# Kernel optimization log

Hardware: AMD Instinct MI355X
Metric: run time of the kernel (lower is better)

The kernel has to match this reference:

```python
import jax, jax.numpy as jnp
import numpy as np

B, D, V = 1024, 512, 100000
M = 0.4
EPS = 1e-07


def setup_inputs() -> dict:
    key = jax.random.key(0)
    k1, k2, k3 = jax.random.split(key, 3)
    inp = jax.random.normal(k1, (B, D), dtype=jnp.float32)
    # xavier_uniform for (D, V): limit = sqrt(6/(D+V))
    limit = float(np.sqrt(6.0 / (D + V)))
    weight = jax.random.uniform(k2, (D, V), dtype=jnp.float32, minval=-limit, maxval=limit)
    labels = jax.random.randint(k3, (B,), 0, V, dtype=jnp.int64)
    return {"input": inp, "weight": weight, "labels": labels}


def reference(input, weight, labels):
    # L2-normalize rows of input and columns of weight (F.normalize eps=1e-12)
    x_norm = input / jnp.maximum(jnp.linalg.norm(input, axis=1, keepdims=True), 1e-12)
    w_norm = weight / jnp.maximum(jnp.linalg.norm(weight, axis=0, keepdims=True), 1e-12)
    cosine = x_norm @ w_norm                                # [B, V]
    cosine = jnp.clip(cosine, -1.0 + EPS, 1.0 - EPS)
    arcos = jnp.arccos(cosine)
    # add margin m only at the label class (one-hot add without dense one-hot)
    rows = jnp.arange(B)
    arcos = arcos.at[rows, labels].add(M)
    logits = jnp.cos(arcos)                                 # [B, V]
    # cross-entropy, mean reduction
    logz = jax.nn.logsumexp(logits, axis=1)                 # [B]
    label_logit = logits[rows, labels]                      # [B]
    loss = jnp.mean(logz - label_logit)
    return loss
```

## Files before the change

kernel.cpp:

```cpp
#include <hip/hip_runtime.h>
#include <math.h>

#define B_    1024
#define D_    512
#define V_    100000
#define NP_   100096
#define NT_   782
#define EPS_  1e-7f
#define COSM  0.9210609940028851f
#define SINM  0.3894183423086505f

typedef __bf16 bf16x8 __attribute__((ext_vector_type(8)));
typedef float  f32x4  __attribute__((ext_vector_type(4)));

struct alignas(16) US8 { unsigned short h[8]; };

__device__ __forceinline__ unsigned short f2bf(float f) {
  union { float f; unsigned u; } a; a.f = f;
  unsigned u = a.u;
  u += 0x7FFFu + ((u >> 16) & 1u);
  return (unsigned short)(u >> 16);
}

__device__ __forceinline__ void async_copy16(void* lds, const void* g) {
  __builtin_amdgcn_global_load_lds(
      (const __attribute__((address_space(1))) void*)g,
      (__attribute__((address_space(3))) void*)lds, 16, 0, 0);
}

__global__ void x_prep(const float* __restrict__ x,
                       unsigned short* __restrict__ xb,
                       float* __restrict__ S) {
  int t = threadIdx.x;
  int lane = t & 63, wave = t >> 6;
  int row = blockIdx.x * 4 + wave;
  const float* xr = x + (size_t)row * D_;
  f32x4 a = *(const f32x4*)(xr + lane * 8);
  f32x4 b = *(const f32x4*)(xr + lane * 8 + 4);
  float ss = a[0]*a[0] + a[1]*a[1] + a[2]*a[2] + a[3]*a[3]
           + b[0]*b[0] + b[1]*b[1] + b[2]*b[2] + b[3]*b[3];
#pragma unroll
  for (int off = 32; off > 0; off >>= 1) ss += __shfl_xor(ss, off, 64);
  float inv = 1.0f / fmaxf(sqrtf(ss), 1e-12f);
  US8 pk;
#pragma unroll
  for (int j = 0; j < 4; ++j) pk.h[j]     = f2bf(a[j] * inv);
#pragma unroll
  for (int j = 0; j < 4; ++j) pk.h[4 + j] = f2bf(b[j] * inv);
  *(US8*)(xb + (size_t)row * D_ + lane * 8) = pk;
  if (lane == 0) S[row] = 0.0f;
}

#define WPC 64
#define KH  256

__global__ __launch_bounds__(256) void w_prep(const float* __restrict__ w,
                                              unsigned short* __restrict__ wbT,
                                              float* __restrict__ wssq) {
  __shared__ US8  T16[WPC][32];
  __shared__ float sq[16][WPC];
  int t = threadIdx.x;
  int c0 = blockIdx.x * WPC;
  int qv = t & 15;
  int rg = t >> 4;
  int colv = qv * 4;
  int lane = t & 63, wave = t >> 6;
  bool vok = (c0 + colv + 3) < V_;
  float ssq[4] = {0.0f, 0.0f, 0.0f, 0.0f};

  for (int h = 0; h < 2; ++h) {
#pragma unroll
    for (int o = 0; o < 2; ++o) {
      int kc = rg * 2 + o;
      int rowb = h * KH + kc * 8;
      US8 pk[4] = {};
      if (vok) {
#pragma unroll
        for (int i = 0; i < 8; ++i) {
          f32x4 v = *(const f32x4*)(w + (size_t)(rowb + i) * V_ + c0 + colv);
#pragma unroll
          for (int cc = 0; cc < 4; ++cc) {
            ssq[cc] += v[cc] * v[cc];
            pk[cc].h[i] = f2bf(v[cc]);
          }
        }
      }
#pragma unroll
      for (int cc = 0; cc < 4; ++cc)
        T16[colv + cc][kc ^ qv] = pk[cc];
    }
    __syncthreads();
#pragma unroll
    for (int ci = 0; ci < 8; ++ci) {
      int col = wave * 16 + ci * 2 + (lane >> 5);
      int kc = lane & 31;
      US8 pk = T16[col][kc ^ (col >> 2)];
      *(US8*)(wbT + (size_t)(c0 + col) * D_ + h * KH + kc * 8) = pk;
    }
    __syncthreads();
  }

#pragma unroll
  for (int cc = 0; cc < 4; ++cc) sq[rg][colv + cc] = ssq[cc];
  __syncthreads();
  if (t < WPC && (c0 + t) < V_) {
    float tot = 0.0f;
#pragma unroll
    for (int p = 0; p < 16; ++p) tot += sq[p][t];
    wssq[c0 + t] = tot;
  }
}

#define BM 256
#define BN 128
#define BK 64
#define NKT (D_ / BK)

__global__ __launch_bounds__(512, 4) void gemm_fused_dma(
    const unsigned short* __restrict__ xb,
    const unsigned short* __restrict__ wbT,
    const float* __restrict__ wssq,
    const int* __restrict__ labels,
    float* __restrict__ S, float* __restrict__ Lb) {
  int bid = blockIdx.x;
  int xcd = bid & 7;
  int slot = bid >> 3;
  int tm = slot & 3;
  int tn = xcd * 98 + (slot >> 2);
  if (tn >= NT_) return;
  int m0 = tm * BM, n0 = tn * BN;

  __shared__ unsigned short Ab[BM * BK];
  __shared__ unsigned short Bb[BN * BK];
  __shared__ int labT[BM];
  int t = threadIdx.x;
  if (t < BM) labT[t] = labels[m0 + t];
  int lane = t & 63;
  int q = lane >> 4, l15 = lane & 15;
  int wave = t >> 6;
  int wm = (wave & 3) * 64, wn = (wave >> 2) * 64;
  f32x4 acc[4][4] = {};

  const unsigned short* gA[4]; unsigned short* lA[4];
  const unsigned short* gB[2]; unsigned short* lB[2];
#pragma unroll
  for (int j = 0; j < 4; ++j) {
    int p = t + 512 * j;
    int m = p >> 3;
    int kc = (p & 7) ^ (m & 7);
    gA[j] = xb + (size_t)(m0 + m) * D_ + kc * 8;
    lA[j] = Ab + p * 8;
  }
#pragma unroll
  for (int j = 0; j < 2; ++j) {
    int p = t + 512 * j;
    int m = p >> 3;
    int kc = (p & 7) ^ (m & 7);
    gB[j] = wbT + (size_t)(n0 + m) * D_ + kc * 8;
    lB[j] = Bb + p * 8;
  }

  int h = l15 & 7;
  for (int kt = 0; kt < D_; kt += BK) {
#pragma unroll
    for (int j = 0; j < 4; ++j) async_copy16(lA[j], gA[j] + kt);
#pragma unroll
    for (int j = 0; j < 2; ++j) async_copy16(lB[j], gB[j] + kt);
    __syncthreads();

#pragma unroll
    for (int s = 0; s < 2; ++s) {
      int kx = s * 4 + q;
      bf16x8 af[4], bfr[4];
#pragma unroll
      for (int ri = 0; ri < 4; ++ri) {
        int row_ = wm + ri * 16 + l15;
        af[ri] = *(const bf16x8*)&Ab[(row_ * 8 + (kx ^ h)) * 8];
      }
#pragma unroll
      for (int ci = 0; ci < 4; ++ci) {
        int row_ = wn + ci * 16 + l15;
        bfr[ci] = *(const bf16x8*)&Bb[(row_ * 8 + (kx ^ h)) * 8];
      }
#pragma unroll
      for (int ri = 0; ri < 4; ++ri)
#pragma unroll
        for (int ci = 0; ci < 4; ++ci)
          acc[ri][ci] = __builtin_amdgcn_mfma_f32_16x16x32_bf16(
              af[ri], bfr[ci], acc[ri][ci], 0, 0, 0);
    }
    __syncthreads();
  }

  float iw[4]; int vcol[4];
#pragma unroll
  for (int ci = 0; ci < 4; ++ci) {
    int nl = wn + ci * 16 + l15;
    vcol[ci] = n0 + nl;
    iw[ci] = (vcol[ci] < V_) ? 1.0f / fmaxf(sqrtf(wssq[vcol[ci]]), 1e-12f)
                             : 0.0f;
  }
#pragma unroll
  for (int ri = 0; ri < 4; ++ri) {
#pragma unroll
    for (int reg = 0; reg < 4; ++reg) {
      int ml = wm + ri * 16 + q * 4 + reg;
      int r = m0 + ml;
      int lab = labT[ml];
      float s = 0.0f;
#pragma unroll
      for (int ci = 0; ci < 4; ++ci) {
        float cv = acc[ri][ci][reg] * iw[ci];
        cv = fminf(fmaxf(cv, -1.0f + EPS_), 1.0f - EPS_);
        float logit = cv;
        if (vcol[ci] == lab) {
          logit = cv * COSM - sqrtf(fmaxf(1.0f - cv * cv, 0.0f)) * SINM;
          Lb[r] = logit;
        }
        s += (vcol[ci] < V_) ? __expf(logit) : 0.0f;
      }
      s += __shfl_xor(s, 1, 64);
      s += __shfl_xor(s, 2, 64);
      s += __shfl_xor(s, 4, 64);
      s += __shfl_xor(s, 8, 64);
      if (l15 == 0) atomicAdd(&S[r], s);
    }
  }
}

__global__ __launch_bounds__(256) void gemm_fused_inline(
    const unsigned short* __restrict__ xb,
    const float* __restrict__ w,
    const int* __restrict__ labels,
    float* __restrict__ S, float* __restrict__ Lb) {
  int bid = blockIdx.x;
  int xcd = bid & 7;
  int slot = bid >> 3;
  int tn = xcd * 98 + (slot >> 3);
  int tm = slot & 7;
  if (tn >= NT_) return;
  int m0 = tm * 128, n0 = tn * 128;

  __shared__ unsigned short Ab[128 * 64];
  __shared__ unsigned short Bb[128 * 64];
  __shared__ float sqred[8][128];
  __shared__ float iwL[128];
  __shared__ int labT[128];
  int t = threadIdx.x;
  if (t < 128) labT[t] = labels[m0 + t];
  int lane = t & 63;
  int q = lane >> 4, l15 = lane & 15;
  int wave = t >> 6;
  int wm = (wave & 1) * 64, wn = (wave >> 1) * 64;
  f32x4 acc[4][4] = {};

  const unsigned short* gA[4];
  unsigned short* lA[4];
#pragma unroll
  for (int j = 0; j < 4; ++j) {
    int p = t + 256 * j;
    int m = p >> 3;
    int kc = (p & 7) ^ (m & 7);
    gA[j] = xb + (size_t)(m0 + m) * D_ + kc * 8;
    lA[j] = Ab + p * 8;
  }

  int cg = t & 31;
  int rp = t >> 5;
  int c0l = cg * 4;
  bool vok = (n0 + c0l + 3) < V_;
  const float* wbase = w + (size_t)rp * 8 * V_ + n0 + c0l;
  unsigned short* bdst[4];
#pragma unroll
  for (int cc = 0; cc < 4; ++cc) {
    int col = c0l + cc;
    bdst[cc] = &Bb[(col * 8 + (rp ^ (col & 7))) * 8];
  }
  float ssq[4] = {0.0f, 0.0f, 0.0f, 0.0f};

  for (int kt = 0; kt < D_; kt += 64) {
#pragma unroll
    for (int j = 0; j < 4; ++j) async_copy16(lA[j], gA[j] + kt);

    f32x4 row[8];
    if (vok) {
#pragma unroll
      for (int i = 0; i < 8; ++i)
        row[i] = *(const f32x4*)(wbase + (size_t)i * V_);
    } else {
#pragma unroll
      for (int i = 0; i < 8; ++i) row[i] = f32x4{0.0f, 0.0f, 0.0f, 0.0f};
    }
#pragma unroll
    for (int cc = 0; cc < 4; ++cc) {
      US8 pk;
#pragma unroll
      for (int i = 0; i < 8; ++i) {
        float v = row[i][cc];
        ssq[cc] += v * v;
        pk.h[i] = f2bf(v);
      }
      *(US8*)bdst[cc] = pk;
    }
    wbase += (size_t)64 * V_;

    __syncthreads();
    int h = l15 & 7;
#pragma unroll
    for (int s = 0; s < 2; ++s) {
      int kx = s * 4 + q;
      bf16x8 af[4], bfr[4];
#pragma unroll
      for (int ri = 0; ri < 4; ++ri) {
        int row_ = wm + ri * 16 + l15;
        af[ri] = *(const bf16x8*)&Ab[(row_ * 8 + (kx ^ h)) * 8];
      }
#pragma unroll
      for (int ci = 0; ci < 4; ++ci) {
        int row_ = wn + ci * 16 + l15;
        bfr[ci] = *(const bf16x8*)&Bb[(row_ * 8 + (kx ^ h)) * 8];
      }
#pragma unroll
      for (int ri = 0; ri < 4; ++ri)
#pragma unroll
        for (int ci = 0; ci < 4; ++ci)
          acc[ri][ci] = __builtin_amdgcn_mfma_f32_16x16x32_bf16(
              af[ri], bfr[ci], acc[ri][ci], 0, 0, 0);
    }
    __syncthreads();
  }

#pragma unroll
  for (int cc = 0; cc < 4; ++cc) sqred[rp][c0l + cc] = ssq[cc];
  __syncthreads();
  if (t < 128) {
    float tot = 0.0f;
#pragma unroll
    for (int p = 0; p < 8; ++p) tot += sqred[p][t];
    iwL[t] = ((n0 + t) < V_) ? 1.0f / fmaxf(sqrtf(tot), 1e-12f) : 0.0f;
  }
  __syncthreads();

  float iw[4]; int vcol[4];
#pragma unroll
  for (int ci = 0; ci < 4; ++ci) {
    int nl = wn + ci * 16 + l15;
    vcol[ci] = n0 + nl;
    iw[ci] = iwL[nl];
  }
#pragma unroll
  for (int ri = 0; ri < 4; ++ri) {
#pragma unroll
    for (int reg = 0; reg < 4; ++reg) {
      int ml = wm + ri * 16 + q * 4 + reg;
      int r = m0 + ml;
      int lab = labT[ml];
      float s = 0.0f;
#pragma unroll
      for (int ci = 0; ci < 4; ++ci) {
        float cv = acc[ri][ci][reg] * iw[ci];
        cv = fminf(fmaxf(cv, -1.0f + EPS_), 1.0f - EPS_);
        float logit = cv;
        if (vcol[ci] == lab) {
          logit = cv * COSM - sqrtf(fmaxf(1.0f - cv * cv, 0.0f)) * SINM;
          Lb[r] = logit;
        }
        s += (vcol[ci] < V_) ? __expf(logit) : 0.0f;
      }
      s += __shfl_xor(s, 1, 64);
      s += __shfl_xor(s, 2, 64);
      s += __shfl_xor(s, 4, 64);
      s += __shfl_xor(s, 8, 64);
      if (l15 == 0) atomicAdd(&S[r], s);
    }
  }
}

__global__ void finalk(const float* __restrict__ S, const float* __restrict__ Lb,
                       float* __restrict__ out) {
  __shared__ float red[256];
  int t = threadIdx.x;
  float s = 0.0f;
  for (int i = t; i < B_; i += 256) s += logf(S[i]) - Lb[i];
  red[t] = s;
  __syncthreads();
  for (int o = 128; o > 0; o >>= 1) {
    if (t < o) red[t] += red[t + o];
    __syncthreads();
  }
  if (t == 0) out[0] = red[0] * (1.0f / B_);
}

extern "C" void kernel_launch(void* const* d_in, const int* in_sizes, int n_in,
                              void* d_out, int out_size, void* d_ws, size_t ws_size,
                              hipStream_t stream) {
  const float* x = (const float*)d_in[0];
  const float* w = (const float*)d_in[1];
  const int* labels = (const int*)d_in[2];
  float* out = (float*)d_out;
  char* ws = (char*)d_ws;
  unsigned short* xb = (unsigned short*)ws;
  float* S    = (float*)(ws + 1048576ull);
  float* Lb   = (float*)(ws + 1052672ull);
  float* wssq = (float*)(ws + 1056768ull);
  unsigned short* wbT = (unsigned short*)(ws + 1457152ull);
  const size_t WS_NEED = 1457152ull + (size_t)NP_ * D_ * 2ull;

  x_prep<<<256, 256, 0, stream>>>(x, xb, S);
  if (ws_size >= WS_NEED) {
    w_prep<<<NP_ / WPC, 256, 0, stream>>>(w, wbT, wssq);
    gemm_fused_dma<<<3136, 512, 0, stream>>>(xb, wbT, wssq, labels, S, Lb);
  } else {
    gemm_fused_inline<<<6272, 256, 0, stream>>>(xb, w, labels, S, Lb);
  }
  finalk<<<1, 256, 0, stream>>>(S, Lb, out);
}
```

Baseline: 494.2 us.

## Double-buffer GEMM LDS tiles with async prefetch and widen w_prep column tile

The fused GEMM now keeps two LDS buffers for the A and B tiles and prefetches the k-tile two steps ahead with async copies. Explicit vmcnt waits and raw barriers replace the single-buffer load-sync-compute loop, so global loads overlap with MFMA work. The labels LDS table is removed in favour of direct global reads, and the launch-bounds occupancy hint is dropped. Separately, w_prep processes 128 columns per block instead of 64. The cost is doubled LDS use (about 96KB per block), which lowers occupancy, plus some extra global label loads.

```diff
diff --git a/kernel.cpp b/kernel.cpp
--- a/kernel.cpp
+++ b/kernel.cpp
@@ -51,28 +51,28 @@
   if (lane == 0) S[row] = 0.0f;
 }
 
-#define WPC 64
+#define WPC 128
 #define KH  256
 
 __global__ __launch_bounds__(256) void w_prep(const float* __restrict__ w,
                                               unsigned short* __restrict__ wbT,
                                               float* __restrict__ wssq) {
   __shared__ US8  T16[WPC][32];
-  __shared__ float sq[16][WPC];
+  __shared__ float sq[8][WPC];
   int t = threadIdx.x;
   int c0 = blockIdx.x * WPC;
-  int qv = t & 15;
-  int rg = t >> 4;
-  int colv = qv * 4;
+  int q32 = t & 31;
+  int rg = t >> 5;
+  int colv = q32 * 4;
   int lane = t & 63, wave = t >> 6;
   bool vok = (c0 + colv + 3) < V_;
   float ssq[4] = {0.0f, 0.0f, 0.0f, 0.0f};
 
   for (int h = 0; h < 2; ++h) {
 #pragma unroll
-    for (int o = 0; o < 2; ++o) {
-      int kc = rg * 2 + o;
-      int rowb = h * KH + kc * 8;
+    for (int m = 0; m < 4; ++m) {
+      int kchunk = rg + m * 8;
+      int rowb = h * KH + kchunk * 8;
       US8 pk[4] = {};
       if (vok) {
 #pragma unroll
@@ -87,12 +87,12 @@
       }
 #pragma unroll
       for (int cc = 0; cc < 4; ++cc)
-        T16[colv + cc][kc ^ qv] = pk[cc];
+        T16[colv + cc][kchunk ^ q32] = pk[cc];
     }
     __syncthreads();
 #pragma unroll
-    for (int ci = 0; ci < 8; ++ci) {
-      int col = wave * 16 + ci * 2 + (lane >> 5);
+    for (int ci = 0; ci < 16; ++ci) {
+      int col = wave * 32 + ci * 2 + (lane >> 5);
       int kc = lane & 31;
       US8 pk = T16[col][kc ^ (col >> 2)];
       *(US8*)(wbT + (size_t)(c0 + col) * D_ + h * KH + kc * 8) = pk;
@@ -106,7 +106,7 @@
   if (t < WPC && (c0 + t) < V_) {
     float tot = 0.0f;
 #pragma unroll
-    for (int p = 0; p < 16; ++p) tot += sq[p][t];
+    for (int p = 0; p < 8; ++p) tot += sq[p][t];
     wssq[c0 + t] = tot;
   }
 }
@@ -116,7 +116,7 @@
 #define BK 64
 #define NKT (D_ / BK)
 
-__global__ __launch_bounds__(512, 4) void gemm_fused_dma(
+__global__ __launch_bounds__(512) void gemm_fused_dma(
     const unsigned short* __restrict__ xb,
     const unsigned short* __restrict__ wbT,
     const float* __restrict__ wssq,
@@ -130,26 +130,24 @@
   if (tn >= NT_) return;
   int m0 = tm * BM, n0 = tn * BN;
 
-  __shared__ unsigned short Ab[BM * BK];
-  __shared__ unsigned short Bb[BN * BK];
-  __shared__ int labT[BM];
+  __shared__ unsigned short Ab[2 * BM * BK];
+  __shared__ unsigned short Bb[2 * BN * BK];
   int t = threadIdx.x;
-  if (t < BM) labT[t] = labels[m0 + t];
   int lane = t & 63;
   int q = lane >> 4, l15 = lane & 15;
   int wave = t >> 6;
   int wm = (wave & 3) * 64, wn = (wave >> 2) * 64;
   f32x4 acc[4][4] = {};
 
-  const unsigned short* gA[4]; unsigned short* lA[4];
-  const unsigned short* gB[2]; unsigned short* lB[2];
+  const unsigned short* gA[4]; int oA[4];
+  const unsigned short* gB[2]; int oB[2];
 #pragma unroll
   for (int j = 0; j < 4; ++j) {
     int p = t + 512 * j;
     int m = p >> 3;
     int kc = (p & 7) ^ (m & 7);
     gA[j] = xb + (size_t)(m0 + m) * D_ + kc * 8;
-    lA[j] = Ab + p * 8;
+    oA[j] = p * 8;
   }
 #pragma unroll
   for (int j = 0; j < 2; ++j) {
@@ -157,17 +155,27 @@
     int m = p >> 3;
     int kc = (p & 7) ^ (m & 7);
     gB[j] = wbT + (size_t)(n0 + m) * D_ + kc * 8;
-    lB[j] = Bb + p * 8;
-  }
+    oB[j] = p * 8;
+  }
+
+#pragma unroll
+  for (int j = 0; j < 4; ++j) async_copy16(Ab + oA[j], gA[j]);
+#pragma unroll
+  for (int j = 0; j < 2; ++j) async_copy16(Bb + oB[j], gB[j]);
+#pragma unroll
+  for (int j = 0; j < 4; ++j) async_copy16(Ab + BM * BK + oA[j], gA[j] + BK);
+#pragma unroll
+  for (int j = 0; j < 2; ++j) async_copy16(Bb + BN * BK + oB[j], gB[j] + BK);
+  asm volatile("s_waitcnt vmcnt(6)" ::: "memory");
+  __builtin_amdgcn_sched_barrier(0);
+  __builtin_amdgcn_s_barrier();
+  __builtin_amdgcn_sched_barrier(0);
 
   int h = l15 & 7;
-  for (int kt = 0; kt < D_; kt += BK) {
-#pragma unroll
-    for (int j = 0; j < 4; ++j) async_copy16(lA[j], gA[j] + kt);
-#pragma unroll
-    for (int j = 0; j < 2; ++j) async_copy16(lB[j], gB[j] + kt);
-    __syncthreads();
-
+  for (int tt = 0; tt < NKT; ++tt) {
+    int b = tt & 1;
+    const unsigned short* Ac = Ab + b * (BM * BK);
+    const unsigned short* Bc = Bb + b * (BN * BK);
 #pragma unroll
     for (int s = 0; s < 2; ++s) {
       int kx = s * 4 + q;
@@ -175,12 +183,12 @@
 #pragma unroll
       for (int ri = 0; ri < 4; ++ri) {
         int row_ = wm + ri * 16 + l15;
-        af[ri] = *(const bf16x8*)&Ab[(row_ * 8 + (kx ^ h)) * 8];
+        af[ri] = *(const bf16x8*)&Ac[(row_ * 8 + (kx ^ h)) * 8];
       }
 #pragma unroll
       for (int ci = 0; ci < 4; ++ci) {
         int row_ = wn + ci * 16 + l15;
-        bfr[ci] = *(const bf16x8*)&Bb[(row_ * 8 + (kx ^ h)) * 8];
+        bfr[ci] = *(const bf16x8*)&Bc[(row_ * 8 + (kx ^ h)) * 8];
       }
 #pragma unroll
       for (int ri = 0; ri < 4; ++ri)
@@ -189,7 +197,24 @@
           acc[ri][ci] = __builtin_amdgcn_mfma_f32_16x16x32_bf16(
               af[ri], bfr[ci], acc[ri][ci], 0, 0, 0);
     }
-    __syncthreads();
+    __builtin_amdgcn_sched_barrier(0);
+    __builtin_amdgcn_s_barrier();
+    __builtin_amdgcn_sched_barrier(0);
+    if (tt + 2 < NKT) {
+      int kk = (tt + 2) * BK;
+#pragma unroll
+      for (int j = 0; j < 4; ++j)
+        async_copy16(Ab + b * (BM * BK) + oA[j], gA[j] + kk);
+#pragma unroll
+      for (int j = 0; j < 2; ++j)
+        async_copy16(Bb + b * (BN * BK) + oB[j], gB[j] + kk);
+      asm volatile("s_waitcnt vmcnt(6)" ::: "memory");
+    } else {
+      asm volatile("s_waitcnt vmcnt(0)" ::: "memory");
+    }
+    __builtin_amdgcn_sched_barrier(0);
+    __builtin_amdgcn_s_barrier();
+    __builtin_amdgcn_sched_barrier(0);
   }
 
   float iw[4]; int vcol[4];
@@ -206,7 +231,7 @@
     for (int reg = 0; reg < 4; ++reg) {
       int ml = wm + ri * 16 + q * 4 + reg;
       int r = m0 + ml;
-      int lab = labT[ml];
+      int lab = labels[r];
       float s = 0.0f;
 #pragma unroll
       for (int ci = 0; ci < 4; ++ci) {
```

New measurement: 581.7 us. +17.7%, slower.
